# Performance work log

Hardware: AMD Instinct MI355X
Metric: run time of the kernel (lower is better)

Reference implementation:

```python
import jax, jax.numpy as jnp
import numpy as np

NUM_GRAPHS = 512


def gcn_conv(x, W, b, src, dst, deg_inv_sqrt, n_nodes):
    # PyG GCNConv: out = D^{-1/2} (A+I) D^{-1/2} X W + b
    h = x @ W                                             # [N, F_out]
    norm = deg_inv_sqrt[src] * deg_inv_sqrt[dst]          # [E]
    msg = h[src] * norm[:, None]                          # gather + scale, [E, F_out]
    agg = jax.ops.segment_sum(msg, dst, num_segments=n_nodes)
    agg = agg + h * (deg_inv_sqrt ** 2)[:, None]          # self-loop term (norm = 1/deg)
    return agg + b


def setup_inputs() -> dict:
    key = jax.random.key(0)
    ks = jax.random.split(key, 8)
    N, E, F_in = 50000, 800000, 256
    hid2, out = 128, 64
    x = jax.random.normal(ks[0], (N, F_in), dtype=jnp.float32)
    edge_index = jax.random.randint(ks[1], (2, E), 0, N, dtype=jnp.int32)
    batch = jnp.sort(jax.random.randint(ks[2], (N,), 0, NUM_GRAPHS, dtype=jnp.int32))
    s = lambda k, sh: jax.random.normal(k, sh, dtype=jnp.float32) * (1.0 / np.sqrt(sh[0]))
    return {
        "x": x,
        "edge_index": edge_index,
        "batch": batch,
        "W1": s(ks[3], (F_in, hid2)), "b1": jnp.zeros((hid2,), jnp.float32),
        "W3": s(ks[4], (hid2, out)), "b3": jnp.zeros((out,), jnp.float32),
        "W4": s(ks[5], (hid2, out)), "b4": jnp.zeros((out,), jnp.float32),
        "Wfc": s(ks[6], (out, 4)), "bfc": jnp.zeros((4,), jnp.float32),
        "noise": jax.random.normal(ks[7], (N, out), dtype=jnp.float32),
    }


def reference(x, edge_index, batch, W1, b1, W3, b3, W4, b4, Wfc, bfc, noise):
    n_nodes = x.shape[0]
    src, dst = edge_index[0], edge_index[1]
    # degree of A + I (count of incoming edges per dst, plus self-loop)
    deg = jax.ops.segment_sum(jnp.ones_like(src, dtype=x.dtype), dst,
                              num_segments=n_nodes) + 1.0
    deg_inv_sqrt = jax.lax.rsqrt(deg)

    h = jax.nn.relu(gcn_conv(x, W1, b1, src, dst, deg_inv_sqrt, n_nodes))  # dropout p=0
    mean = gcn_conv(h, W3, b3, src, dst, deg_inv_sqrt, n_nodes)
    log_std = gcn_conv(h, W4, b4, src, dst, deg_inv_sqrt, n_nodes)
    z = mean + noise * jnp.exp(log_std)                   # reparametrize (training=True)

    # scatter_mean over graph ids
    sums = jax.ops.segment_sum(z, batch, num_segments=NUM_GRAPHS)
    counts = jax.ops.segment_sum(jnp.ones((n_nodes,), z.dtype), batch,
                                 num_segments=NUM_GRAPHS)
    pooled = sums / jnp.maximum(counts, 1.0)[:, None]     # [G, out]

    logits = pooled @ Wfc + bfc                           # [G, 4]
    return jax.nn.log_softmax(logits, axis=1)
```

## Files before the change

kernel.cpp:

```cpp
#include <hip/hip_runtime.h>
#include <hip/hip_bf16.h>
#include <cstdint>
#include <cmath>


__device__ __forceinline__ unsigned short f2bf(float f) {
    union { float f; unsigned u; } v; v.f = f;
    unsigned u = v.u;
    return (unsigned short)((u + 0x7fffu + ((u >> 16) & 1u)) >> 16);
}
__device__ __forceinline__ float bf2f(unsigned b) {
    union { float f; unsigned u; } v; v.u = b << 16; return v.f;
}
__device__ __forceinline__ unsigned packbf(float lo, float hi) {
    return (unsigned)f2bf(lo) | ((unsigned)f2bf(hi) << 16);
}

__global__ __launch_bounds__(256) void deg_kernel(const int* __restrict__ dst,
                                                  int* __restrict__ deg, int E) {
    int e = blockIdx.x * 256 + threadIdx.x;
    if (e < E) atomicAdd(&deg[dst[e]], 1);
}

__global__ __launch_bounds__(256) void scan1_kernel(const int* __restrict__ deg,
                                                    int* __restrict__ bsum, int N) {
    int t = threadIdx.x;
    int base = blockIdx.x * 1024 + t * 4;
    int s = 0;
    if (base + 3 < N) {
        int4 v = *(const int4*)(deg + base);
        s = v.x + v.y + v.z + v.w;
    } else {
        for (int i = 0; i < 4; i++) if (base + i < N) s += deg[base + i];
    }
    __shared__ int red[256];
    red[t] = s;
    __syncthreads();
    for (int off = 128; off > 0; off >>= 1) {
        if (t < off) red[t] += red[t + off];
        __syncthreads();
    }
    if (t == 0) bsum[blockIdx.x] = red[0];
}

__global__ __launch_bounds__(256) void scan2_kernel(int* __restrict__ bsum, int nb) {
    __shared__ int s[256];
    int t = threadIdx.x;
    s[t] = (t < nb) ? bsum[t] : 0;
    __syncthreads();
    for (int off = 1; off < 256; off <<= 1) {
        int u = (t >= off) ? s[t - off] : 0;
        __syncthreads();
        s[t] += u;
        __syncthreads();
    }
    if (t < nb) bsum[t] = (t == 0) ? 0 : s[t - 1];
}

__global__ __launch_bounds__(256) void scan3_kernel(const int* __restrict__ deg,
                                                    const int* __restrict__ bsum,
                                                    int* __restrict__ offs,
                                                    int* __restrict__ cursor,
                                                    float* __restrict__ dis,
                                                    int N, int E) {
    int t = threadIdx.x;
    int bid = blockIdx.x;
    int base = bid * 1024 + t * 4;
    int d[4] = {0, 0, 0, 0};
    if (base + 3 < N) {
        int4 v = *(const int4*)(deg + base);
        d[0] = v.x; d[1] = v.y; d[2] = v.z; d[3] = v.w;
    } else {
        for (int i = 0; i < 4; i++) if (base + i < N) d[i] = deg[base + i];
    }
    int s = d[0] + d[1] + d[2] + d[3];
    __shared__ int red[256];
    red[t] = s;
    __syncthreads();
    for (int off = 1; off < 256; off <<= 1) {
        int u = (t >= off) ? red[t - off] : 0;
        __syncthreads();
        red[t] += u;
        __syncthreads();
    }
    int run = bsum[bid] + ((t == 0) ? 0 : red[t - 1]);
#pragma unroll
    for (int i = 0; i < 4; i++) {
        int idx = base + i;
        if (idx < N) {
            offs[idx] = run;
            cursor[idx] = run;
            dis[idx] = rsqrtf((float)d[i] + 1.0f);
            run += d[i];
        }
    }
    if (bid == 0 && t == 0) offs[N] = E;
}

__global__ __launch_bounds__(256) void fill_kernel(const int* __restrict__ src,
                                                   const int* __restrict__ dst,
                                                   int* __restrict__ cursor,
                                                   int* __restrict__ adj, int E) {
    int e = blockIdx.x * 256 + threadIdx.x;
    if (e >= E) return;
    int pos = atomicAdd(&cursor[dst[e]], 1);
    adj[pos] = src[e];
}

__global__ __launch_bounds__(256) void gemm1_kernel(const float* __restrict__ x,
                                                    const float* __restrict__ W,
                                                    const float* __restrict__ dis,
                                                    unsigned short* __restrict__ Abf,
                                                    float* __restrict__ B, int N) {
    __shared__ float xs[64][68];
    __shared__ float ws[64][128];
    int tid = threadIdx.x;
    int tx = tid & 15;
    int ty = tid >> 4;
    int rowBase = blockIdx.x * 64;

    float acc[4][8];
#pragma unroll
    for (int i = 0; i < 4; i++)
#pragma unroll
        for (int j = 0; j < 8; j++) acc[i][j] = 0.f;

    for (int k0 = 0; k0 < 256; k0 += 64) {
#pragma unroll
        for (int i = 0; i < 4; i++) {
            int u = tid + i * 256;
            int r = u >> 4;
            int c = u & 15;
            float4 v = make_float4(0.f, 0.f, 0.f, 0.f);
            int row = rowBase + r;
            if (row < N) v = *(const float4*)(x + (size_t)row * 256 + k0 + c * 4);
            *(float4*)&xs[r][c * 4] = v;
        }
#pragma unroll
        for (int i = 0; i < 8; i++) {
            int u = tid + i * 256;
            int r = u >> 5;
            int c = u & 31;
            *(float4*)&ws[r][c * 4] = *(const float4*)(W + (size_t)(k0 + r) * 128 + c * 4);
        }
        __syncthreads();
#pragma unroll
        for (int k = 0; k < 64; k++) {
            float xv[4];
#pragma unroll
            for (int i = 0; i < 4; i++) xv[i] = xs[ty * 4 + i][k];
            float4 w0 = *(float4*)&ws[k][tx * 4];
            float4 w1 = *(float4*)&ws[k][64 + tx * 4];
            float wv[8] = {w0.x, w0.y, w0.z, w0.w, w1.x, w1.y, w1.z, w1.w};
#pragma unroll
            for (int i = 0; i < 4; i++)
#pragma unroll
                for (int j = 0; j < 8; j++) acc[i][j] = fmaf(xv[i], wv[j], acc[i][j]);
        }
        __syncthreads();
    }
#pragma unroll
    for (int i = 0; i < 4; i++) {
        int row = rowBase + ty * 4 + i;
        if (row >= N) continue;
        float dv = dis[row];
        float d2 = dv * dv;
#pragma unroll
        for (int half = 0; half < 2; half++) {
            int colBase = half * 64 + tx * 4;
            float4 v = make_float4(acc[i][half * 4], acc[i][half * 4 + 1],
                                   acc[i][half * 4 + 2], acc[i][half * 4 + 3]);
            ushort4 a4;
            a4.x = f2bf(v.x * dv); a4.y = f2bf(v.y * dv);
            a4.z = f2bf(v.z * dv); a4.w = f2bf(v.w * dv);
            *(ushort4*)(Abf + (size_t)row * 128 + colBase) = a4;
            float4 b = make_float4(v.x * d2, v.y * d2, v.z * d2, v.w * d2);
            *(float4*)(B + (size_t)row * 128 + colBase) = b;
        }
    }
}

template <int MODE>
__global__ __launch_bounds__(256) void gather_kernel(const int* __restrict__ offs,
                                                     const int* __restrict__ adj,
                                                     const float* __restrict__ dis,
                                                     const float* __restrict__ b1,
                                                     const unsigned short* __restrict__ Ain,
                                                     unsigned short* __restrict__ Aout,
                                                     float* __restrict__ B, int N) {
    int tid = threadIdx.x;
    int lane = tid & 15;
    int node = blockIdx.x * 16 + (tid >> 4);
    if (node >= N) return;
    int beg = offs[node];
    int end = offs[node + 1];
    float a[8];
#pragma unroll
    for (int j = 0; j < 8; j++) a[j] = 0.f;
    int e = beg;
    for (; e + 3 < end; e += 4) {
        int s0 = adj[e], s1 = adj[e + 1], s2 = adj[e + 2], s3 = adj[e + 3];
        uint4 r0 = ((const uint4*)(Ain + (size_t)s0 * 128))[lane];
        uint4 r1 = ((const uint4*)(Ain + (size_t)s1 * 128))[lane];
        uint4 r2 = ((const uint4*)(Ain + (size_t)s2 * 128))[lane];
        uint4 r3 = ((const uint4*)(Ain + (size_t)s3 * 128))[lane];
        a[0] += bf2f(r0.x & 0xffffu) + bf2f(r1.x & 0xffffu) + bf2f(r2.x & 0xffffu) + bf2f(r3.x & 0xffffu);
        a[1] += bf2f(r0.x >> 16)     + bf2f(r1.x >> 16)     + bf2f(r2.x >> 16)     + bf2f(r3.x >> 16);
        a[2] += bf2f(r0.y & 0xffffu) + bf2f(r1.y & 0xffffu) + bf2f(r2.y & 0xffffu) + bf2f(r3.y & 0xffffu);
        a[3] += bf2f(r0.y >> 16)     + bf2f(r1.y >> 16)     + bf2f(r2.y >> 16)     + bf2f(r3.y >> 16);
        a[4] += bf2f(r0.z & 0xffffu) + bf2f(r1.z & 0xffffu) + bf2f(r2.z & 0xffffu) + bf2f(r3.z & 0xffffu);
        a[5] += bf2f(r0.z >> 16)     + bf2f(r1.z >> 16)     + bf2f(r2.z >> 16)     + bf2f(r3.z >> 16);
        a[6] += bf2f(r0.w & 0xffffu) + bf2f(r1.w & 0xffffu) + bf2f(r2.w & 0xffffu) + bf2f(r3.w & 0xffffu);
        a[7] += bf2f(r0.w >> 16)     + bf2f(r1.w >> 16)     + bf2f(r2.w >> 16)     + bf2f(r3.w >> 16);
    }
    for (; e < end; e++) {
        int s = adj[e];
        uint4 r0 = ((const uint4*)(Ain + (size_t)s * 128))[lane];
        a[0] += bf2f(r0.x & 0xffffu);
        a[1] += bf2f(r0.x >> 16);
        a[2] += bf2f(r0.y & 0xffffu);
        a[3] += bf2f(r0.y >> 16);
        a[4] += bf2f(r0.z & 0xffffu);
        a[5] += bf2f(r0.z >> 16);
        a[6] += bf2f(r0.w & 0xffffu);
        a[7] += bf2f(r0.w >> 16);
    }
    float dd = dis[node];
    float* brow = B + (size_t)node * 128 + lane * 8;
    float4 cur0 = *(float4*)brow;
    float4 cur1 = *(float4*)(brow + 4);
    if (MODE == 0) {
        cur0.x += dd * a[0]; cur0.y += dd * a[1]; cur0.z += dd * a[2]; cur0.w += dd * a[3];
        cur1.x += dd * a[4]; cur1.y += dd * a[5]; cur1.z += dd * a[6]; cur1.w += dd * a[7];
        *(float4*)brow = cur0;
        *(float4*)(brow + 4) = cur1;
    } else {
        const float* b1p = b1 + lane * 8;
        float4 bb0 = *(const float4*)b1p;
        float4 bb1 = *(const float4*)(b1p + 4);
        float v0 = fmaxf(cur0.x + dd * a[0] + bb0.x, 0.f);
        float v1 = fmaxf(cur0.y + dd * a[1] + bb0.y, 0.f);
        float v2 = fmaxf(cur0.z + dd * a[2] + bb0.z, 0.f);
        float v3 = fmaxf(cur0.w + dd * a[3] + bb0.w, 0.f);
        float v4 = fmaxf(cur1.x + dd * a[4] + bb1.x, 0.f);
        float v5 = fmaxf(cur1.y + dd * a[5] + bb1.y, 0.f);
        float v6 = fmaxf(cur1.z + dd * a[6] + bb1.z, 0.f);
        float v7 = fmaxf(cur1.w + dd * a[7] + bb1.w, 0.f);
        uint4 w;
        w.x = packbf(v0 * dd, v1 * dd);
        w.y = packbf(v2 * dd, v3 * dd);
        w.z = packbf(v4 * dd, v5 * dd);
        w.w = packbf(v6 * dd, v7 * dd);
        *(uint4*)(Aout + (size_t)node * 128 + lane * 8) = w;
        float d2 = dd * dd;
        *(float4*)brow       = make_float4(v0 * d2, v1 * d2, v2 * d2, v3 * d2);
        *(float4*)(brow + 4) = make_float4(v4 * d2, v5 * d2, v6 * d2, v7 * d2);
    }
}

__device__ __forceinline__ int lbound_lds(const int* a, int n, int v) {
    int l = 0, r = n;
    while (l < r) { int m = (l + r) >> 1; if (a[m] < v) l = m + 1; else r = m; }
    return l;
}

__global__ __launch_bounds__(256) void pool2_kernel(const float* __restrict__ hagg,
                                                    const float* __restrict__ W4,
                                                    const float* __restrict__ b4,
                                                    const float* __restrict__ noise,
                                                    const int* __restrict__ batch,
                                                    float* __restrict__ pooledH,
                                                    float* __restrict__ pooledT,
                                                    int N) {
    __shared__ float xs[64][132];
    __shared__ float ws[128][64];
    __shared__ int sbatch[64];
    int tid = threadIdx.x;
    int rowBase = blockIdx.x * 64;
    int nrows = min(64, N - rowBase);

#pragma unroll
    for (int i = 0; i < 32; i++)
        ((float4*)ws)[tid + i * 256] = ((const float4*)W4)[tid + i * 256];
#pragma unroll
    for (int i = 0; i < 8; i++) {
        int u = tid + i * 256;
        int r = u >> 5;
        int c = u & 31;
        int row = rowBase + r;
        float4 v = make_float4(0.f, 0.f, 0.f, 0.f);
        if (row < N) v = *(const float4*)(hagg + (size_t)row * 128 + c * 4);
        *(float4*)&xs[r][c * 4] = v;
    }
    if (tid < 64) {
        int row = rowBase + tid;
        sbatch[tid] = (row < N) ? batch[row] : 0x7fffffff;
    }
    __syncthreads();

    int tx = tid & 15;
    int ty = tid >> 4;
    float acc[4][4];
#pragma unroll
    for (int i = 0; i < 4; i++)
#pragma unroll
        for (int j = 0; j < 4; j++) acc[i][j] = 0.f;
#pragma unroll 8
    for (int k = 0; k < 128; k++) {
        float xv[4];
#pragma unroll
        for (int i = 0; i < 4; i++) xv[i] = xs[ty * 4 + i][k];
        float4 wv = *(float4*)&ws[k][tx * 4];
        float w[4] = {wv.x, wv.y, wv.z, wv.w};
#pragma unroll
        for (int i = 0; i < 4; i++)
#pragma unroll
            for (int j = 0; j < 4; j++) acc[i][j] = fmaf(xv[i], w[j], acc[i][j]);
    }
    __syncthreads();

    int g0 = sbatch[0];
    int g1 = (nrows > 0) ? sbatch[nrows - 1] : g0;

    for (int g = g0; g <= g1; g++) {
        int lo = lbound_lds(sbatch, nrows, g);
        int hi = lbound_lds(sbatch, nrows, g + 1);
        if (hi > lo && tid < 128) {
            float s = 0.f;
            for (int r = lo; r < hi; r++) s += xs[r][tid];
            atomicAdd(&pooledH[g * 128 + tid], s);
        }
    }
    __syncthreads();

    float4 b4v = *(const float4*)(b4 + tx * 4);
    float bb[4] = {b4v.x, b4v.y, b4v.z, b4v.w};
#pragma unroll
    for (int i = 0; i < 4; i++) {
        int row = rowBase + ty * 4 + i;
        if (row < N) {
            float4 nz = *(const float4*)(noise + (size_t)row * 64 + tx * 4);
            float nv[4] = {nz.x, nz.y, nz.z, nz.w};
#pragma unroll
            for (int j = 0; j < 4; j++)
                xs[ty * 4 + i][tx * 4 + j] = nv[j] * expf(acc[i][j] + bb[j]);
        }
    }
    __syncthreads();

    for (int g = g0; g <= g1; g++) {
        int lo = lbound_lds(sbatch, nrows, g);
        int hi = lbound_lds(sbatch, nrows, g + 1);
        if (hi > lo && tid < 64) {
            float s = 0.f;
            for (int r = lo; r < hi; r++) s += xs[r][tid];
            atomicAdd(&pooledT[g * 64 + tid], s);
        }
    }
}

__global__ __launch_bounds__(64) void final_kernel(const float* __restrict__ pooledH,
                                                   const float* __restrict__ pooledT,
                                                   const int* __restrict__ batch,
                                                   const float* __restrict__ W3,
                                                   const float* __restrict__ b3,
                                                   const float* __restrict__ Wfc,
                                                   const float* __restrict__ bfc,
                                                   float* __restrict__ out, int N) {
    int g = blockIdx.x;
    int f = threadIdx.x;
    __shared__ int seg[2];
    if (f < 2) {
        int target = g + f;
        int l = 0, r = N;
        while (l < r) { int m = (l + r) >> 1; if (batch[m] < target) l = m + 1; else r = m; }
        seg[f] = l;
    }
    __syncthreads();
    float cnt = (float)(seg[1] - seg[0]);
    float denom = fmaxf(cnt, 1.0f);
    float p = pooledT[g * 64 + f] + cnt * b3[f];
    const float* ph = pooledH + g * 128;
#pragma unroll
    for (int k = 0; k < 128; k++) p = fmaf(ph[k], W3[k * 64 + f], p);
    p /= denom;
    __shared__ float pl[64];
    __shared__ float lg[4];
    pl[f] = p;
    __syncthreads();
    if (f < 4) {
        float l = bfc[f];
#pragma unroll
        for (int k = 0; k < 64; k++) l = fmaf(pl[k], Wfc[k * 4 + f], l);
        lg[f] = l;
    }
    __syncthreads();
    if (f == 0) {
        float m = fmaxf(fmaxf(lg[0], lg[1]), fmaxf(lg[2], lg[3]));
        float s = expf(lg[0] - m) + expf(lg[1] - m) + expf(lg[2] - m) + expf(lg[3] - m);
        float lse = logf(s);
#pragma unroll
        for (int j = 0; j < 4; j++) out[g * 4 + j] = lg[j] - m - lse;
    }
}

extern "C" void kernel_launch(void* const* d_in, const int* in_sizes, int n_in,
                              void* d_out, int out_size, void* d_ws, size_t ws_size,
                              hipStream_t stream) {
    const float* x     = (const float*)d_in[0];
    const int*   ei    = (const int*)d_in[1];
    const int*   batch = (const int*)d_in[2];
    const float* W1    = (const float*)d_in[3];
    const float* b1    = (const float*)d_in[4];
    const float* W3    = (const float*)d_in[5];
    const float* b3    = (const float*)d_in[6];
    const float* W4    = (const float*)d_in[7];
    const float* b4    = (const float*)d_in[8];
    const float* Wfc   = (const float*)d_in[9];
    const float* bfc   = (const float*)d_in[10];
    const float* noise = (const float*)d_in[11];
    float* out = (float*)d_out;

    int N = in_sizes[0] / 256;
    int E = in_sizes[1] / 2;
    const int* src = ei;
    const int* dst = ei + E;
    int nScanBlocks = (N + 1023) / 1024;

    float* B = (float*)d_ws;
    unsigned short* Abf = (unsigned short*)(B + (size_t)N * 128);
    float* dis     = (float*)(Abf + (size_t)N * 128);
    float* pooledH = dis + N;
    float* pooledT = pooledH + 512 * 128;
    int*   degi    = (int*)(pooledT + 512 * 64);
    int*   offs    = degi + N;
    int*   cursor  = offs + N + 1;
    int*   bsum    = cursor + N;
    int*   adj     = bsum + 256;

    hipMemsetAsync(degi, 0, (size_t)N * sizeof(int), stream);
    hipMemsetAsync(pooledH, 0, (size_t)(512 * 128 + 512 * 64) * sizeof(float), stream);

    deg_kernel<<<(E + 255) / 256, 256, 0, stream>>>(dst, degi, E);
    scan1_kernel<<<nScanBlocks, 256, 0, stream>>>(degi, bsum, N);
    scan2_kernel<<<1, 256, 0, stream>>>(bsum, nScanBlocks);
    scan3_kernel<<<nScanBlocks, 256, 0, stream>>>(degi, bsum, offs, cursor, dis, N, E);
    fill_kernel<<<(E + 255) / 256, 256, 0, stream>>>(src, dst, cursor, adj, E);

    gemm1_kernel<<<(N + 63) / 64, 256, 0, stream>>>(x, W1, dis, Abf, B, N);

    gather_kernel<1><<<(N + 15) / 16, 256, 0, stream>>>(offs, adj, dis, b1, Abf, Abf, B, N);

    gather_kernel<0><<<(N + 15) / 16, 256, 0, stream>>>(offs, adj, dis, b1, Abf, Abf, B, N);

    pool2_kernel<<<(N + 63) / 64, 256, 0, stream>>>(B, W4, b4, noise, batch,
                                                    pooledH, pooledT, N);

    final_kernel<<<512, 64, 0, stream>>>(pooledH, pooledT, batch, W3, b3, Wfc, bfc, out, N);
}
```

Baseline: 369.3 us.

## Use bf16 MFMA for the first GCN layer GEMM

Replaces the FP32 FMA tiled GEMM for x@W1 with a bf16 MFMA kernel. A new small kernel converts and transposes W1 to bf16, and each block converts a 64-row x tile to bf16 in shared memory before issuing 16x16x32 MFMAs. The aim is to cut the compute cost of the largest dense matmul. In exchange it adds bf16 rounding of the inputs, one extra kernel launch, and narrower scalar epilogue stores.

After: 343.8 us. 6.9% less time.

```diff
diff --git a/kernel.cpp b/kernel.cpp
--- a/kernel.cpp
+++ b/kernel.cpp
@@ -3,6 +3,9 @@
 #include <cstdint>
 #include <cmath>
 
+
+typedef __attribute__((ext_vector_type(8))) short bf16x8;
+typedef __attribute__((ext_vector_type(4))) float f32x4;
 
 __device__ __forceinline__ unsigned short f2bf(float f) {
     union { float f; unsigned u; } v; v.f = f;
@@ -107,75 +110,82 @@
     adj[pos] = src[e];
 }
 
-__global__ __launch_bounds__(256) void gemm1_kernel(const float* __restrict__ x,
-                                                    const float* __restrict__ W,
-                                                    const float* __restrict__ dis,
-                                                    unsigned short* __restrict__ Abf,
-                                                    float* __restrict__ B, int N) {
-    __shared__ float xs[64][68];
-    __shared__ float ws[64][128];
+__global__ __launch_bounds__(256) void wt_kernel(const float* __restrict__ W,
+                                                 unsigned short* __restrict__ wT) {
+    int idx = blockIdx.x * 256 + threadIdx.x;
+    if (idx < 32768) {
+        int k = idx >> 7;
+        int c = idx & 127;
+        wT[c * 256 + k] = f2bf(W[idx]);
+    }
+}
+
+__global__ __launch_bounds__(256) void gemm1_mfma(const float* __restrict__ x,
+                                                  const unsigned short* __restrict__ wT,
+                                                  const float* __restrict__ dis,
+                                                  unsigned short* __restrict__ Abf,
+                                                  float* __restrict__ B, int N) {
+    __shared__ unsigned short xs[64 * 264];
     int tid = threadIdx.x;
-    int tx = tid & 15;
-    int ty = tid >> 4;
     int rowBase = blockIdx.x * 64;
-
-    float acc[4][8];
-#pragma unroll
-    for (int i = 0; i < 4; i++)
-#pragma unroll
-        for (int j = 0; j < 8; j++) acc[i][j] = 0.f;
-
-    for (int k0 = 0; k0 < 256; k0 += 64) {
-#pragma unroll
-        for (int i = 0; i < 4; i++) {
-            int u = tid + i * 256;
-            int r = u >> 4;
-            int c = u & 15;
-            float4 v = make_float4(0.f, 0.f, 0.f, 0.f);
-            int row = rowBase + r;
-            if (row < N) v = *(const float4*)(x + (size_t)row * 256 + k0 + c * 4);
-            *(float4*)&xs[r][c * 4] = v;
-        }
-#pragma unroll
-        for (int i = 0; i < 8; i++) {
-            int u = tid + i * 256;
-            int r = u >> 5;
-            int c = u & 31;
-            *(float4*)&ws[r][c * 4] = *(const float4*)(W + (size_t)(k0 + r) * 128 + c * 4);
-        }
-        __syncthreads();
-#pragma unroll
-        for (int k = 0; k < 64; k++) {
-            float xv[4];
-#pragma unroll
-            for (int i = 0; i < 4; i++) xv[i] = xs[ty * 4 + i][k];
-            float4 w0 = *(float4*)&ws[k][tx * 4];
-            float4 w1 = *(float4*)&ws[k][64 + tx * 4];
-            float wv[8] = {w0.x, w0.y, w0.z, w0.w, w1.x, w1.y, w1.z, w1.w};
-#pragma unroll
-            for (int i = 0; i < 4; i++)
-#pragma unroll
-                for (int j = 0; j < 8; j++) acc[i][j] = fmaf(xv[i], wv[j], acc[i][j]);
-        }
-        __syncthreads();
-    }
-#pragma unroll
-    for (int i = 0; i < 4; i++) {
-        int row = rowBase + ty * 4 + i;
-        if (row >= N) continue;
-        float dv = dis[row];
-        float d2 = dv * dv;
-#pragma unroll
-        for (int half = 0; half < 2; half++) {
-            int colBase = half * 64 + tx * 4;
-            float4 v = make_float4(acc[i][half * 4], acc[i][half * 4 + 1],
-                                   acc[i][half * 4 + 2], acc[i][half * 4 + 3]);
-            ushort4 a4;
-            a4.x = f2bf(v.x * dv); a4.y = f2bf(v.y * dv);
-            a4.z = f2bf(v.z * dv); a4.w = f2bf(v.w * dv);
-            *(ushort4*)(Abf + (size_t)row * 128 + colBase) = a4;
-            float4 b = make_float4(v.x * d2, v.y * d2, v.z * d2, v.w * d2);
-            *(float4*)(B + (size_t)row * 128 + colBase) = b;
+#pragma unroll
+    for (int i = 0; i < 16; i++) {
+        int u = tid + i * 256;
+        int r = u >> 6;
+        int c = u & 63;
+        float4 v = make_float4(0.f, 0.f, 0.f, 0.f);
+        int row = rowBase + r;
+        if (row < N) v = *(const float4*)(x + (size_t)row * 256 + c * 4);
+        ushort4 b;
+        b.x = f2bf(v.x); b.y = f2bf(v.y); b.z = f2bf(v.z); b.w = f2bf(v.w);
+        *(ushort4*)&xs[r * 264 + c * 4] = b;
+    }
+    __syncthreads();
+
+    int wv = tid >> 6;
+    int l = tid & 63;
+    int lr = l & 15;
+    int lk = l >> 4;
+    int colBase = wv * 32;
+
+    f32x4 acc[4][2];
+#pragma unroll
+    for (int rt = 0; rt < 4; rt++)
+#pragma unroll
+        for (int ct = 0; ct < 2; ct++) acc[rt][ct] = (f32x4){0.f, 0.f, 0.f, 0.f};
+
+    for (int ks = 0; ks < 8; ks++) {
+        int kbase = ks * 32 + lk * 8;
+        bf16x8 a[4], b[2];
+#pragma unroll
+        for (int rt = 0; rt < 4; rt++)
+            a[rt] = *(const bf16x8*)&xs[(rt * 16 + lr) * 264 + kbase];
+#pragma unroll
+        for (int ct = 0; ct < 2; ct++)
+            b[ct] = *(const bf16x8*)(wT + (size_t)(colBase + ct * 16 + lr) * 256 + kbase);
+#pragma unroll
+        for (int rt = 0; rt < 4; rt++)
+#pragma unroll
+            for (int ct = 0; ct < 2; ct++)
+                acc[rt][ct] = __builtin_amdgcn_mfma_f32_16x16x32_bf16(
+                    a[rt], b[ct], acc[rt][ct], 0, 0, 0);
+    }
+
+#pragma unroll
+    for (int rt = 0; rt < 4; rt++) {
+#pragma unroll
+        for (int j = 0; j < 4; j++) {
+            int row = rowBase + rt * 16 + lk * 4 + j;
+            if (row >= N) continue;
+            float dv = dis[row];
+            float d2 = dv * dv;
+#pragma unroll
+            for (int ct = 0; ct < 2; ct++) {
+                int col = colBase + ct * 16 + lr;
+                float v = acc[rt][ct][j];
+                Abf[(size_t)row * 128 + col] = f2bf(v * dv);
+                B[(size_t)row * 128 + col] = v * d2;
+            }
         }
     }
 }
@@ -429,7 +439,8 @@
 
     float* B = (float*)d_ws;
     unsigned short* Abf = (unsigned short*)(B + (size_t)N * 128);
-    float* dis     = (float*)(Abf + (size_t)N * 128);
+    unsigned short* wT  = Abf + (size_t)N * 128;
+    float* dis     = (float*)(wT + 128 * 256);
     float* pooledH = dis + N;
     float* pooledT = pooledH + 512 * 128;
     int*   degi    = (int*)(pooledT + 512 * 64);
@@ -446,8 +457,9 @@
     scan2_kernel<<<1, 256, 0, stream>>>(bsum, nScanBlocks);
     scan3_kernel<<<nScanBlocks, 256, 0, stream>>>(degi, bsum, offs, cursor, dis, N, E);
     fill_kernel<<<(E + 255) / 256, 256, 0, stream>>>(src, dst, cursor, adj, E);
-
-    gemm1_kernel<<<(N + 63) / 64, 256, 0, stream>>>(x, W1, dis, Abf, B, N);
+    wt_kernel<<<128, 256, 0, stream>>>(W1, wT);
+
+    gemm1_mfma<<<(N + 63) / 64, 256, 0, stream>>>(x, wT, dis, Abf, B, N);
 
     gather_kernel<1><<<(N + 15) / 16, 256, 0, stream>>>(offs, adj, dis, b1, Abf, Abf, B, N);
 
```
